# Performance work log

Measured on AMD Instinct MI355X. Metric: run time of the kernel, lower is better.

## Reference

```python
import jax, jax.numpy as jnp
import numpy as np

IN_C, HID_C, OUT_C = 128, 256, 128
N_NODES, N_EDGES = 50000, 600000


def setup_inputs() -> dict:
    key = jax.random.key(0)
    ks = jax.random.split(key, 8)
    x = jax.random.normal(ks[0], (N_NODES, IN_C), dtype=jnp.float32)
    edge_index = jax.random.randint(ks[1], (2, N_EDGES), 0, N_NODES, dtype=jnp.int64)
    def glorot(k, shape):
        lim = np.sqrt(6.0 / (shape[0] + shape[1])).astype(np.float32)
        return jax.random.uniform(k, shape, dtype=jnp.float32, minval=-lim, maxval=lim)
    # PyG SAGEConv: out = lin_l(mean_aggr) + lin_r(x_root); bias only in lin_l
    W1_l = glorot(ks[2], (IN_C, HID_C)); b1 = jnp.zeros((HID_C,), jnp.float32)
    W1_r = glorot(ks[3], (IN_C, HID_C))
    W2_l = glorot(ks[4], (HID_C, OUT_C)); b2 = jnp.zeros((OUT_C,), jnp.float32)
    W2_r = glorot(ks[5], (HID_C, OUT_C))
    return {"x": x, "edge_index": edge_index, "W1_l": W1_l, "b1": b1, "W1_r": W1_r,
            "W2_l": W2_l, "b2": b2, "W2_r": W2_r}


def _sage_conv(x, src, dst, W_l, b, W_r):
    n = x.shape[0]
    msg = x[src]  # [E, C] gather from source nodes
    agg = jax.ops.segment_sum(msg, dst, num_segments=n)
    cnt = jax.ops.segment_sum(jnp.ones((src.shape[0],), x.dtype), dst, num_segments=n)
    agg = agg / jnp.maximum(cnt, 1.0)[:, None]  # mean aggregation, zero-deg safe
    return agg @ W_l + b + x @ W_r


def reference(x, edge_index, W1_l, b1, W1_r, W2_l, b2, W2_r):
    src, dst = edge_index[0], edge_index[1]
    h = jax.nn.relu(_sage_conv(x, src, dst, W1_l, b1, W1_r))
    return _sage_conv(h, src, dst, W2_l, b2, W2_r)
```

## Files before the change

kernel.cpp:

```cpp
#include <hip/hip_runtime.h>
#include <hip/hip_bf16.h>


#define N_NODES 50000
#define IN_C    128
#define HID_C   256
#define OUT_C   128
#define N_EDGES 600000

#define PB_ZERO 196
#define PB_W1   (PB_ZERO + 256)
#define PB_W2   (PB_W1 + 256)
#define PB_X    (PB_W2 + 6250)

typedef __attribute__((ext_vector_type(8))) short short8;
typedef __attribute__((ext_vector_type(4))) float f32x4;

__device__ __forceinline__ float bf2f(short s) {
    union { unsigned u; float f; } c;
    c.u = ((unsigned)(unsigned short)s) << 16;
    return c.f;
}

__global__ __launch_bounds__(256) void prep(
    const float* __restrict__ x, __hip_bfloat16* __restrict__ A1,
    const float* __restrict__ W1l, const float* __restrict__ W1r,
    const float* __restrict__ W2l, const float* __restrict__ W2r,
    __hip_bfloat16* __restrict__ W1t, __hip_bfloat16* __restrict__ W2t,
    int* __restrict__ cnt, int* __restrict__ total) {
    int b = blockIdx.x;
    if (b < PB_ZERO) {
        int i = b * 256 + threadIdx.x;
        if (i < N_NODES) cnt[i] = 0;
        if (b == 0 && threadIdx.x == 0) *total = 0;
    } else if (b < PB_W1) {
        int reg = b - PB_ZERO;
        int half = reg >> 7;
        int t = (reg & 127) * 256 + threadIdx.x;
        int k = t >> 8, n = t & 255;
        const float* src = half ? W1r : W1l;
        W1t[n * 256 + half * 128 + k] = __float2bfloat16(src[t]);
    } else if (b < PB_W2) {
        int reg = b - PB_W1;
        int half = reg >> 7;
        int t = (reg & 127) * 256 + threadIdx.x;
        int k = t >> 7, n = t & 127;
        const float* src = half ? W2r : W2l;
        W2t[(size_t)(half * 128 + n) * 256 + k] = __float2bfloat16(src[t]);
    } else {
        int t = (b - PB_W2) * 256 + threadIdx.x;
        if (t >= N_NODES * 32) return;
        int row = t >> 5, c = (t & 31) * 4;
        float4 v = *(const float4*)(x + (size_t)row * 128 + c);
        __hip_bfloat16* d = A1 + (size_t)row * 256 + 128 + c;
        __hip_bfloat162 p0, p1;
        p0.x = __float2bfloat16(v.x); p0.y = __float2bfloat16(v.y);
        p1.x = __float2bfloat16(v.z); p1.y = __float2bfloat16(v.w);
        *(__hip_bfloat162*)d = p0;
        *(__hip_bfloat162*)(d + 2) = p1;
    }
}


__global__ void count_deg(const int* __restrict__ dst, int* __restrict__ cnt, int E) {
    int e = blockIdx.x * blockDim.x + threadIdx.x;
    if (e < E) atomicAdd(&cnt[dst[e]], 1);
}

__global__ __launch_bounds__(256) void assign_offsets(
    const int* __restrict__ cnt, int* __restrict__ row_ptr,
    int* __restrict__ cursor, int* __restrict__ total, int n) {
    __shared__ int tmp[256];
    __shared__ int sbase;
    int t = threadIdx.x, g = blockIdx.x * 256 + t;
    int v = (g < n) ? cnt[g] : 0;
    tmp[t] = v; __syncthreads();
    for (int off = 1; off < 256; off <<= 1) {
        int u = (t >= off) ? tmp[t - off] : 0;
        __syncthreads();
        tmp[t] += u;
        __syncthreads();
    }
    if (t == 255) sbase = atomicAdd(total, tmp[255]);
    __syncthreads();
    if (g < n) {
        int e = sbase + tmp[t] - v;
        row_ptr[g] = e;
        cursor[g] = e;
    }
}

__global__ void fill_csr(const int* __restrict__ srcI, const int* __restrict__ dstI,
                         int* __restrict__ cursor, int* __restrict__ col, int E) {
    int e = blockIdx.x * blockDim.x + threadIdx.x;
    if (e < E) {
        int pos = atomicAdd(&cursor[dstI[e]], 1);
        col[pos] = srcI[e];
    }
}

template <int FINAL>
__global__ __launch_bounds__(256) void aggregate_mean(
    const __hip_bfloat16* __restrict__ feat, int featStride,
    const int* __restrict__ row_ptr, const int* __restrict__ deg,
    const int* __restrict__ col,
    void* __restrict__ outp, int outStride,
    const float* __restrict__ pre, int nNodes) {
    int node = blockIdx.x * 16 + (threadIdx.x >> 4);
    int sl   = threadIdx.x & 15;
    if (node >= nNodes) return;
    int beg = row_ptr[node];
    int d   = deg[node];
    const __hip_bfloat16* base = feat + sl * 8;
    float a[8];
    #pragma unroll
    for (int c = 0; c < 8; ++c) a[c] = 0.f;
    int j = 0;
    for (; j + 4 <= d; j += 4) {
        int s0 = col[beg + j];
        int s1 = col[beg + j + 1];
        int s2 = col[beg + j + 2];
        int s3 = col[beg + j + 3];
        short8 v0 = *(const short8*)(base + (size_t)s0 * featStride);
        short8 v1 = *(const short8*)(base + (size_t)s1 * featStride);
        short8 v2 = *(const short8*)(base + (size_t)s2 * featStride);
        short8 v3 = *(const short8*)(base + (size_t)s3 * featStride);
        #pragma unroll
        for (int c = 0; c < 8; ++c)
            a[c] += (bf2f(v0[c]) + bf2f(v1[c])) + (bf2f(v2[c]) + bf2f(v3[c]));
    }
    for (; j < d; ++j) {
        short8 v = *(const short8*)(base + (size_t)col[beg + j] * featStride);
        #pragma unroll
        for (int c = 0; c < 8; ++c) a[c] += bf2f(v[c]);
    }
    float inv = 1.f / (float)max(d, 1);
    #pragma unroll
    for (int c = 0; c < 8; ++c) a[c] *= inv;
    if (FINAL) {
        const float* pp = pre + (size_t)node * 128 + sl * 8;
        float* op = (float*)outp + (size_t)node * 128 + sl * 8;
        float4 p0 = *(const float4*)pp;
        float4 p1 = *(const float4*)(pp + 4);
        *(float4*)op       = make_float4(a[0] + p0.x, a[1] + p0.y, a[2] + p0.z, a[3] + p0.w);
        *(float4*)(op + 4) = make_float4(a[4] + p1.x, a[5] + p1.y, a[6] + p1.z, a[7] + p1.w);
    } else {
        __hip_bfloat16* o = (__hip_bfloat16*)outp + (size_t)node * outStride + sl * 8;
        short8 q;
        #pragma unroll
        for (int c = 0; c < 8; ++c) {
            union { __hip_bfloat16 b; short s; } cv;
            cv.b = __float2bfloat16(a[c]);
            q[c] = cv.s;
        }
        *(short8*)o = q;
    }
}


#define GBM 128
#define GBN 128
#define GBK 64

__device__ __forceinline__ void gload16(const void* g, void* l) {
    typedef const __attribute__((address_space(1))) unsigned int* gp_t;
    typedef __attribute__((address_space(3))) unsigned int* lp_t;
    __builtin_amdgcn_global_load_lds((gp_t)g, (lp_t)l, 16, 0, 0);
}

__global__ __launch_bounds__(256) void gemm_mfma(
    const __hip_bfloat16* __restrict__ A, int lda,
    const __hip_bfloat16* __restrict__ Bt,
    const float* __restrict__ bias,
    __hip_bfloat16* __restrict__ outBf, int outBfStride,
    float* __restrict__ outF,
    int M, int K, int mode) {
    __shared__ __hip_bfloat16 Als[GBM * GBK];
    __shared__ __hip_bfloat16 Bls[GBN * GBK];

    int tid  = threadIdx.x;
    int wave = tid >> 6, lane = tid & 63;
    int wm = wave >> 1, wn = wave & 1;
    int mb = blockIdx.x * GBM, nb = blockIdx.y * GBN;

    int srow_base = wave * 32;
    int lrow = lane >> 3;
    int pch  = lane & 7;

    f32x4 acc[4][4];
    #pragma unroll
    for (int i = 0; i < 4; ++i)
        #pragma unroll
        for (int j = 0; j < 4; ++j)
            acc[i][j] = (f32x4){0.f, 0.f, 0.f, 0.f};

    for (int kt = 0; kt < K; kt += GBK) {
        #pragma unroll
        for (int t = 0; t < 4; ++t) {
            int rloc = srow_base + t * 8 + lrow;
            int lch  = pch ^ (rloc & 7);
            int ga_row = mb + rloc; if (ga_row >= M) ga_row = M - 1;
            const __hip_bfloat16* ga = A + (size_t)ga_row * lda + kt + lch * 8;
            gload16(ga, &Als[(srow_base + t * 8) * GBK]);
            const __hip_bfloat16* gb = Bt + (size_t)(nb + rloc) * K + kt + lch * 8;
            gload16(gb, &Bls[(srow_base + t * 8) * GBK]);
        }
        __syncthreads();

        #pragma unroll
        for (int ks = 0; ks < GBK; ks += 32) {
            int chunkL = (ks >> 3) + (lane >> 4);
            short8 af[4], bf[4];
            #pragma unroll
            for (int i = 0; i < 4; ++i) {
                int row = wm * 64 + i * 16 + (lane & 15);
                int pc  = chunkL ^ (row & 7);
                af[i] = *(const short8*)&Als[row * GBK + pc * 8];
            }
            #pragma unroll
            for (int j = 0; j < 4; ++j) {
                int row = wn * 64 + j * 16 + (lane & 15);
                int pc  = chunkL ^ (row & 7);
                bf[j] = *(const short8*)&Bls[row * GBK + pc * 8];
            }
            #pragma unroll
            for (int i = 0; i < 4; ++i)
                #pragma unroll
                for (int j = 0; j < 4; ++j)
                    acc[i][j] = __builtin_amdgcn_mfma_f32_16x16x32_bf16(
                        af[i], bf[j], acc[i][j], 0, 0, 0);
        }
        __syncthreads();
    }

    int cn[4];
    float bc[4];
    #pragma unroll
    for (int j = 0; j < 4; ++j) {
        cn[j] = wn * 64 + j * 16 + (lane & 15);
        bc[j] = 0.f;
    }
    if (mode == 0) {
        #pragma unroll
        for (int j = 0; j < 4; ++j) bc[j] = bias[nb + cn[j]];
        #pragma unroll
        for (int i = 0; i < 4; ++i)
            #pragma unroll
            for (int r = 0; r < 4; ++r) {
                int row = mb + wm * 64 + i * 16 + (lane >> 4) * 4 + r;
                if (row >= M) continue;
                #pragma unroll
                for (int j = 0; j < 4; ++j) {
                    float v = fmaxf(acc[i][j][r] + bc[j], 0.f);
                    outBf[(size_t)row * outBfStride + nb + cn[j]] = __float2bfloat16(v);
                }
            }
    } else if (blockIdx.y == 0) {
        #pragma unroll
        for (int i = 0; i < 4; ++i)
            #pragma unroll
            for (int r = 0; r < 4; ++r) {
                int row = mb + wm * 64 + i * 16 + (lane >> 4) * 4 + r;
                if (row >= M) continue;
                #pragma unroll
                for (int j = 0; j < 4; ++j)
                    outBf[(size_t)row * 128 + cn[j]] = __float2bfloat16(acc[i][j][r]);
            }
    } else {
        #pragma unroll
        for (int j = 0; j < 4; ++j) bc[j] = bias[cn[j]];
        #pragma unroll
        for (int i = 0; i < 4; ++i)
            #pragma unroll
            for (int r = 0; r < 4; ++r) {
                int row = mb + wm * 64 + i * 16 + (lane >> 4) * 4 + r;
                if (row >= M) continue;
                #pragma unroll
                for (int j = 0; j < 4; ++j)
                    outF[(size_t)row * 128 + cn[j]] = acc[i][j][r] + bc[j];
            }
    }
}

extern "C" void kernel_launch(void* const* d_in, const int* in_sizes, int n_in,
                              void* d_out, int out_size, void* d_ws, size_t ws_size,
                              hipStream_t stream) {
    const float* x    = (const float*)d_in[0];
    const int*   ei   = (const int*)d_in[1];
    const float* W1l  = (const float*)d_in[2];
    const float* b1   = (const float*)d_in[3];
    const float* W1r  = (const float*)d_in[4];
    const float* W2l  = (const float*)d_in[5];
    const float* b2   = (const float*)d_in[6];
    const float* W2r  = (const float*)d_in[7];
    float* out = (float*)d_out;

    const int E = N_EDGES;
    const int N = N_NODES;
    const int* srcI = ei;
    const int* dstI = ei + E;

    char* w = (char*)d_ws;
    int*            cnt     = (int*)(w + 0);
    int*            row_ptr = (int*)(w + 204800);
    int*            col     = (int*)(w + 409600);
    int*            total   = (int*)(w + 2809856);
    __hip_bfloat16* W1t     = (__hip_bfloat16*)(w + 2818048);
    __hip_bfloat16* W2t     = (__hip_bfloat16*)(w + 2949120);
    int*            cursor  = (int*)(w + 3080192);
    __hip_bfloat16* A1      = (__hip_bfloat16*)(w + 3280896);
    __hip_bfloat16* h_bf    = (__hip_bfloat16*)(w + 28880896);
    __hip_bfloat16* hp_bf   = (__hip_bfloat16*)(w + 54480896);
    float*          pre     = (float*)(w + 67280896);

    prep<<<PB_X, 256, 0, stream>>>(x, A1, W1l, W1r, W2l, W2r, W1t, W2t, cnt, total);

    count_deg<<<(E + 255) / 256, 256, 0, stream>>>(dstI, cnt, E);
    assign_offsets<<<(N + 255) / 256, 256, 0, stream>>>(cnt, row_ptr, cursor, total, N);
    fill_csr<<<(E + 255) / 256, 256, 0, stream>>>(srcI, dstI, cursor, col, E);

    aggregate_mean<0><<<(N + 15) / 16, 256, 0, stream>>>(
        A1 + 128, 256, row_ptr, cnt, col, (void*)A1, 256, nullptr, N);
    {
        dim3 grid((N + GBM - 1) / GBM, HID_C / GBN);
        gemm_mfma<<<grid, 256, 0, stream>>>(A1, 256, W1t, b1,
                                            h_bf, 256, nullptr, N, 256, 0);
    }

    {
        dim3 grid((N + GBM - 1) / GBM, 2);
        gemm_mfma<<<grid, 256, 0, stream>>>(h_bf, 256, W2t, b2,
                                            hp_bf, 128, pre, N, 256, 1);
    }
    aggregate_mean<1><<<(N + 15) / 16, 256, 0, stream>>>(
        hp_bf, 128, row_ptr, cnt, col, (void*)out, 128, pre, N);
}
```

Baseline: 245.2 us.

## Fuse degree counting into prep kernel and software-pipeline aggregation gathers

```diff
diff --git a/kernel.cpp b/kernel.cpp
--- a/kernel.cpp
+++ b/kernel.cpp
@@ -8,8 +8,8 @@
 #define OUT_C   128
 #define N_EDGES 600000
 
-#define PB_ZERO 196
-#define PB_W1   (PB_ZERO + 256)
+#define PB_CNT  2344
+#define PB_W1   (PB_CNT + 256)
 #define PB_W2   (PB_W1 + 256)
 #define PB_X    (PB_W2 + 6250)
 
@@ -27,14 +27,13 @@
     const float* __restrict__ W1l, const float* __restrict__ W1r,
     const float* __restrict__ W2l, const float* __restrict__ W2r,
     __hip_bfloat16* __restrict__ W1t, __hip_bfloat16* __restrict__ W2t,
-    int* __restrict__ cnt, int* __restrict__ total) {
+    const int* __restrict__ dstI, int* __restrict__ cnt) {
     int b = blockIdx.x;
-    if (b < PB_ZERO) {
-        int i = b * 256 + threadIdx.x;
-        if (i < N_NODES) cnt[i] = 0;
-        if (b == 0 && threadIdx.x == 0) *total = 0;
+    if (b < PB_CNT) {
+        int e = b * 256 + threadIdx.x;
+        if (e < N_EDGES) atomicAdd(&cnt[dstI[e]], 1);
     } else if (b < PB_W1) {
-        int reg = b - PB_ZERO;
+        int reg = b - PB_CNT;
         int half = reg >> 7;
         int t = (reg & 127) * 256 + threadIdx.x;
         int k = t >> 8, n = t & 255;
@@ -61,12 +60,6 @@
     }
 }
 
-
-__global__ void count_deg(const int* __restrict__ dst, int* __restrict__ cnt, int E) {
-    int e = blockIdx.x * blockDim.x + threadIdx.x;
-    if (e < E) atomicAdd(&cnt[dst[e]], 1);
-}
-
 __global__ __launch_bounds__(256) void assign_offsets(
     const int* __restrict__ cnt, int* __restrict__ row_ptr,
     int* __restrict__ cursor, int* __restrict__ total, int n) {
@@ -115,25 +108,53 @@
     float a[8];
     #pragma unroll
     for (int c = 0; c < 8; ++c) a[c] = 0.f;
+
+    short8 v0, v1, v2, v3;
     int j = 0;
-    for (; j + 4 <= d; j += 4) {
-        int s0 = col[beg + j];
-        int s1 = col[beg + j + 1];
-        int s2 = col[beg + j + 2];
-        int s3 = col[beg + j + 3];
-        short8 v0 = *(const short8*)(base + (size_t)s0 * featStride);
-        short8 v1 = *(const short8*)(base + (size_t)s1 * featStride);
-        short8 v2 = *(const short8*)(base + (size_t)s2 * featStride);
-        short8 v3 = *(const short8*)(base + (size_t)s3 * featStride);
+    if (d >= 4) {
+        int s0 = col[beg + 0], s1 = col[beg + 1];
+        int s2 = col[beg + 2], s3 = col[beg + 3];
+        v0 = *(const short8*)(base + (size_t)s0 * featStride);
+        v1 = *(const short8*)(base + (size_t)s1 * featStride);
+        v2 = *(const short8*)(base + (size_t)s2 * featStride);
+        v3 = *(const short8*)(base + (size_t)s3 * featStride);
+        for (; j + 8 <= d; j += 4) {
+            int t0 = col[beg + j + 4], t1 = col[beg + j + 5];
+            int t2 = col[beg + j + 6], t3 = col[beg + j + 7];
+            short8 w0 = *(const short8*)(base + (size_t)t0 * featStride);
+            short8 w1 = *(const short8*)(base + (size_t)t1 * featStride);
+            short8 w2 = *(const short8*)(base + (size_t)t2 * featStride);
+            short8 w3 = *(const short8*)(base + (size_t)t3 * featStride);
+            #pragma unroll
+            for (int c = 0; c < 8; ++c)
+                a[c] += (bf2f(v0[c]) + bf2f(v1[c])) + (bf2f(v2[c]) + bf2f(v3[c]));
+            v0 = w0; v1 = w1; v2 = w2; v3 = w3;
+        }
         #pragma unroll
         for (int c = 0; c < 8; ++c)
             a[c] += (bf2f(v0[c]) + bf2f(v1[c])) + (bf2f(v2[c]) + bf2f(v3[c]));
-    }
-    for (; j < d; ++j) {
-        short8 v = *(const short8*)(base + (size_t)col[beg + j] * featStride);
-        #pragma unroll
-        for (int c = 0; c < 8; ++c) a[c] += bf2f(v[c]);
-    }
+        j += 4;
+    }
+    int rem = d - j;
+    if (rem > 0) {
+        int s0 = col[beg + j];
+        int s1 = (rem > 1) ? col[beg + j + 1] : s0;
+        int s2 = (rem > 2) ? col[beg + j + 2] : s0;
+        short8 t0 = *(const short8*)(base + (size_t)s0 * featStride);
+        short8 t1 = *(const short8*)(base + (size_t)s1 * featStride);
+        short8 t2 = *(const short8*)(base + (size_t)s2 * featStride);
+        #pragma unroll
+        for (int c = 0; c < 8; ++c) a[c] += bf2f(t0[c]);
+        if (rem > 1) {
+            #pragma unroll
+            for (int c = 0; c < 8; ++c) a[c] += bf2f(t1[c]);
+        }
+        if (rem > 2) {
+            #pragma unroll
+            for (int c = 0; c < 8; ++c) a[c] += bf2f(t2[c]);
+        }
+    }
+
     float inv = 1.f / (float)max(d, 1);
     #pragma unroll
     for (int c = 0; c < 8; ++c) a[c] *= inv;
@@ -302,9 +323,9 @@
 
     char* w = (char*)d_ws;
     int*            cnt     = (int*)(w + 0);
+    int*            total   = (int*)(w + 200000);
     int*            row_ptr = (int*)(w + 204800);
     int*            col     = (int*)(w + 409600);
-    int*            total   = (int*)(w + 2809856);
     __hip_bfloat16* W1t     = (__hip_bfloat16*)(w + 2818048);
     __hip_bfloat16* W2t     = (__hip_bfloat16*)(w + 2949120);
     int*            cursor  = (int*)(w + 3080192);
@@ -313,9 +334,9 @@
     __hip_bfloat16* hp_bf   = (__hip_bfloat16*)(w + 54480896);
     float*          pre     = (float*)(w + 67280896);
 
-    prep<<<PB_X, 256, 0, stream>>>(x, A1, W1l, W1r, W2l, W2r, W1t, W2t, cnt, total);
-
-    count_deg<<<(E + 255) / 256, 256, 0, stream>>>(dstI, cnt, E);
+    hipMemsetAsync(cnt, 0, 200004, stream);
+    prep<<<PB_X, 256, 0, stream>>>(x, A1, W1l, W1r, W2l, W2r, W1t, W2t, dstI, cnt);
+
     assign_offsets<<<(N + 255) / 256, 256, 0, stream>>>(cnt, row_ptr, cursor, total, N);
     fill_csr<<<(E + 255) / 256, 256, 0, stream>>>(srcI, dstI, cursor, col, E);
 
```

New measurement: 243.3 us. No clear change (-0.8%).
